# Kernel tuning notes

Hardware: AMD Instinct MI355X
Metric: run time of the kernel (lower is better)

The kernel has to match this reference:

```python
import jax, jax.numpy as jnp
import numpy as np

NUM_EXPERTS = 8
TOP_K = 2
HIDDEN = 2048
INTER = 7168
NUM_TOKENS = 8192


def setup_inputs() -> dict:
    key = jax.random.key(0)
    k0, k1, k2, k3, k4 = jax.random.split(key, 5)
    hidden_states = jax.random.normal(k0, (NUM_TOKENS, HIDDEN), dtype=jnp.float32)
    gate_w = jax.random.normal(k1, (NUM_EXPERTS, HIDDEN), dtype=jnp.float32) / 10.0
    w1 = jax.random.normal(k2, (NUM_EXPERTS, INTER, HIDDEN), dtype=jnp.float32) / 10.0
    w3 = jax.random.normal(k3, (NUM_EXPERTS, INTER, HIDDEN), dtype=jnp.float32) / 10.0
    w2 = jax.random.normal(k4, (NUM_EXPERTS, HIDDEN, INTER), dtype=jnp.float32) / 10.0
    return {"hidden_states": hidden_states, "gate_w": gate_w, "w1": w1, "w3": w3, "w2": w2}


def reference(hidden_states, gate_w, w1, w3, w2):
    x = hidden_states  # [T, H]
    num_experts = gate_w.shape[0]
    # router
    router_logits = x @ gate_w.T  # [T, E]
    probs = jax.nn.softmax(router_logits.astype(jnp.float32), axis=-1)
    top_w, top_i = jax.lax.top_k(probs, TOP_K)              # [T, K]
    top_w = top_w / jnp.sum(top_w, axis=-1, keepdims=True)  # renormalize
    top_w = top_w.astype(x.dtype)
    # dense [T, E] routing weight (0 for unselected experts)
    expert_ids = jnp.arange(num_experts)
    w_dense = jnp.sum(
        jnp.where(top_i[:, :, None] == expert_ids[None, None, :], top_w[:, :, None], 0.0),
        axis=1,
    )  # [T, E]
    out = jnp.zeros_like(x)
    for e in range(num_experts):
        g = jax.nn.silu(x @ w1[e].T) * (x @ w3[e].T)  # [T, I]
        out = out + w_dense[:, e:e + 1] * (g @ w2[e].T)
    return out
```

## Files before the change

### kernel.cpp

```cpp
#include <hip/hip_runtime.h>

#define NTOK 8192
#define HID 2048
#define ITR 7168
#define NE 8
#define BK32 32
#define TILE32 (128 * BK32)

typedef __attribute__((ext_vector_type(8))) short short8;
typedef __attribute__((ext_vector_type(8))) __bf16 bf16x8;
typedef __attribute__((ext_vector_type(4))) float f32x4;

__device__ __forceinline__ unsigned short f2bf(float f) {
  unsigned int u = __float_as_uint(f);
  u += 0x7FFFu + ((u >> 16) & 1u);
  return (unsigned short)(u >> 16);
}

__device__ __forceinline__ f32x4 mfma_bf16(short8 a, short8 b, f32x4 c) {
  union U { short8 s; bf16x8 b; };
  U ua; ua.s = a;
  U ub; ub.s = b;
  return __builtin_amdgcn_mfma_f32_16x16x32_bf16(ua.b, ub.b, c, 0, 0, 0);
}

typedef __attribute__((address_space(1))) const unsigned int g_u32;
typedef __attribute__((address_space(3))) unsigned int l_u32;

__device__ __forceinline__ void gload16(const unsigned short* src, unsigned short* dst) {
  __builtin_amdgcn_global_load_lds((g_u32*)src, (l_u32*)dst, 16, 0, 0);
}

__device__ __forceinline__ short8 read_frag32(const unsigned short* base, int row, int kelem) {
  int slot = ((row << 2) + (kelem >> 3)) ^ (row & 7);
  return *reinterpret_cast<const short8*>(reinterpret_cast<const char*>(base) + slot * 16);
}

__device__ __forceinline__ void slot_src(int s, int* row, int* c) {
  int r0 = ((s >> 2) ^ (s >> 4)) & 1;
  *row = ((s >> 2) & ~1) | r0;
  *c = ((s ^ r0) & 1) | ((((s >> 1) ^ (s >> 3)) & 1) << 1);
}

#define VMCNT(N) asm volatile("s_waitcnt vmcnt(" #N ")" ::: "memory")
#define BARRIER()                         \
  do {                                    \
    __builtin_amdgcn_s_barrier();         \
    asm volatile("" ::: "memory");        \
  } while (0)

__global__ __launch_bounds__(256) void moe_router(
    const float* __restrict__ x, const float* __restrict__ gw,
    int* __restrict__ cnt, int* __restrict__ pair_token, float* __restrict__ pair_w,
    int4* __restrict__ tok_ep) {
  int wave = threadIdx.x >> 6;
  int lane = threadIdx.x & 63;
  int t = blockIdx.x * 4 + wave;
  const float4* xr = reinterpret_cast<const float4*>(x + (size_t)t * HID);
  float acc[NE];
#pragma unroll
  for (int e = 0; e < NE; ++e) acc[e] = 0.f;
#pragma unroll
  for (int j = 0; j < 8; ++j) {
    int c = lane + 64 * j;
    float4 xv = xr[c];
#pragma unroll
    for (int e = 0; e < NE; ++e) {
      float4 gv = reinterpret_cast<const float4*>(gw + (size_t)e * HID)[c];
      acc[e] += xv.x * gv.x + xv.y * gv.y + xv.z * gv.z + xv.w * gv.w;
    }
  }
#pragma unroll
  for (int e = 0; e < NE; ++e) {
    float s = acc[e];
#pragma unroll
    for (int m = 32; m > 0; m >>= 1) s += __shfl_xor(s, m);
    acc[e] = s;
  }
  if (lane == 0) {
    int e0 = 0; float l0 = acc[0];
#pragma unroll
    for (int e = 1; e < NE; ++e) if (acc[e] > l0) { l0 = acc[e]; e0 = e; }
    int e1 = -1; float l1 = -3.0e38f;
#pragma unroll
    for (int e = 0; e < NE; ++e) if (e != e0 && acc[e] > l1) { l1 = acc[e]; e1 = e; }
    float z = __expf(l1 - l0);
    float w0 = 1.f / (1.f + z);
    float w1 = z / (1.f + z);
    int p0 = atomicAdd(&cnt[e0], 1);
    pair_token[e0 * NTOK + p0] = t;
    pair_w[e0 * NTOK + p0] = w0;
    int p1 = atomicAdd(&cnt[e1], 1);
    pair_token[e1 * NTOK + p1] = t;
    pair_w[e1 * NTOK + p1] = w1;
    tok_ep[t] = make_int4(e0, e1, p0, p1);
  }
}

__global__ void moe_scan(const int* __restrict__ cnt, int* __restrict__ base) {
  if (threadIdx.x == 0) {
    int s = 0;
#pragma unroll
    for (int e = 0; e < NE; ++e) { base[e] = s; s += cnt[e]; }
  }
}

__global__ __launch_bounds__(256) void moe_cvt(const float* __restrict__ src,
                                               unsigned short* __restrict__ dst) {
  size_t i = (size_t)blockIdx.x * 256 + threadIdx.x;
  const float4* p = reinterpret_cast<const float4*>(src) + i * 2;
  float4 a = p[0], b = p[1];
  union { unsigned short us[8]; short8 v; } u;
  u.us[0] = f2bf(a.x); u.us[1] = f2bf(a.y); u.us[2] = f2bf(a.z); u.us[3] = f2bf(a.w);
  u.us[4] = f2bf(b.x); u.us[5] = f2bf(b.y); u.us[6] = f2bf(b.z); u.us[7] = f2bf(b.w);
  reinterpret_cast<short8*>(dst)[i] = u.v;
}


__global__ __launch_bounds__(256, 2) void moe_gemm1_e(
    const unsigned short* __restrict__ xb, const unsigned short* __restrict__ w1b,
    const unsigned short* __restrict__ w3b, const int* __restrict__ cnt,
    const int* __restrict__ base, const int* __restrict__ pair_token,
    unsigned short* __restrict__ g) {
  int e = blockIdx.z;
  int n_e = cnt[e];
  int rowTile = blockIdx.x;
  if (rowTile * 128 >= n_e) return;
  int colTile = blockIdx.y;

  __shared__ unsigned short lds[3 * 3 * TILE32];

  int tid = threadIdx.x;
  int lane = tid & 63;
  int wv = tid >> 6;
  int wr = wv >> 1, wc = wv & 1;
  int lr = lane & 15;
  int lk = (lane >> 4) * 8;

  int slotP = e * NTOK + rowTile * 128;
  int slotG = base[e] + rowTile * 128;
  const unsigned short* w1e = w1b + (size_t)e * ITR * HID + (size_t)colTile * 128 * HID;
  const unsigned short* w3e = w3b + (size_t)e * ITR * HID + (size_t)colTile * 128 * HID;

  const unsigned short* a_s[2];
  const unsigned short* b1_s[2];
  const unsigned short* b3_s[2];
#pragma unroll
  for (int i = 0; i < 2; ++i) {
    int s = wv * 128 + i * 64 + lane;
    int row, c;
    slot_src(s, &row, &c);
    int tok = pair_token[slotP + ((rowTile * 128 + row < n_e) ? row : 0)];
    a_s[i] = xb + (size_t)tok * HID + c * 8;
    b1_s[i] = w1e + (size_t)row * HID + c * 8;
    b3_s[i] = w3e + (size_t)row * HID + c * 8;
  }

  f32x4 acc1[4][4], acc3[4][4];
#pragma unroll
  for (int m = 0; m < 4; ++m)
#pragma unroll
    for (int n = 0; n < 4; ++n) {
      acc1[m][n] = (f32x4){0.f, 0.f, 0.f, 0.f};
      acc3[m][n] = (f32x4){0.f, 0.f, 0.f, 0.f};
    }

#define STAGE1(buf, koff)                                                        \
  do {                                                                           \
    unsigned short* Lb = lds + (buf) * 3 * TILE32 + wv * 1024;                   \
    _Pragma("unroll") for (int i = 0; i < 2; ++i) {                              \
      gload16(a_s[i] + (koff), Lb + i * 512);                                    \
      gload16(b1_s[i] + (koff), Lb + TILE32 + i * 512);                          \
      gload16(b3_s[i] + (koff), Lb + 2 * TILE32 + i * 512);                      \
    }                                                                            \
  } while (0)

  const int nt = HID / BK32;
  STAGE1(0, 0);
  STAGE1(1, BK32);

  for (int t = 0; t < nt; ++t) {
    if (t + 1 < nt) VMCNT(6); else VMCNT(0);
    BARRIER();

    const unsigned short* A = lds + (t % 3) * 3 * TILE32;
    const unsigned short* B1 = A + TILE32;
    const unsigned short* B3 = A + 2 * TILE32;
    short8 av[4];
#pragma unroll
    for (int m = 0; m < 4; ++m) av[m] = read_frag32(A, wr * 64 + m * 16 + lr, lk);
#pragma unroll
    for (int n = 0; n < 4; ++n) {
      short8 b1v = read_frag32(B1, wc * 64 + n * 16 + lr, lk);
      short8 b3v = read_frag32(B3, wc * 64 + n * 16 + lr, lk);
#pragma unroll
      for (int m = 0; m < 4; ++m) {
        acc1[m][n] = mfma_bf16(av[m], b1v, acc1[m][n]);
        acc3[m][n] = mfma_bf16(av[m], b3v, acc3[m][n]);
      }
    }

    if (t + 2 < nt) STAGE1((t + 2) % 3, (t + 2) * BK32);
  }
#undef STAGE1

#pragma unroll
  for (int m = 0; m < 4; ++m) {
    int rbase = wr * 64 + m * 16 + ((lane >> 4) << 2);
#pragma unroll
    for (int r = 0; r < 4; ++r) {
      int rt = rbase + r;
      if (rowTile * 128 + rt < n_e) {
        unsigned short* grow = g + (size_t)(slotG + rt) * ITR + colTile * 128 + wc * 64;
#pragma unroll
        for (int n = 0; n < 4; ++n) {
          float h1 = acc1[m][n][r], h3 = acc3[m][n][r];
          float sl = h1 / (1.f + __expf(-h1));
          grow[n * 16 + lr] = f2bf(sl * h3);
        }
      }
    }
  }
}

__global__ __launch_bounds__(256, 2) void moe_gemm2_k(
    const unsigned short* __restrict__ g, const unsigned short* __restrict__ w2b,
    const int* __restrict__ cnt, const int* __restrict__ base,
    const float* __restrict__ pair_w, float* __restrict__ part) {
  int e = blockIdx.z;
  int n_e = cnt[e];
  int rowTile = blockIdx.x;
  if (rowTile * 128 >= n_e) return;
  int colTile = blockIdx.y;

  __shared__ unsigned short lds[3 * 3 * TILE32];

  int tid = threadIdx.x;
  int lane = tid & 63;
  int wv = tid >> 6;
  int wr = wv >> 1, wc = wv & 1;
  int lr = lane & 15;
  int lk = (lane >> 4) * 8;

  int slotP = e * NTOK + rowTile * 128;
  int slotG = base[e] + rowTile * 128;
  const unsigned short* w2e = w2b + (size_t)e * HID * ITR + (size_t)colTile * 256 * ITR;

  const unsigned short* a_s[2];
  const unsigned short* b0_s[2];
  const unsigned short* b1_s[2];
#pragma unroll
  for (int i = 0; i < 2; ++i) {
    int s = wv * 128 + i * 64 + lane;
    int row, c;
    slot_src(s, &row, &c);
    int rclamp = (rowTile * 128 + row < n_e) ? row : 0;
    a_s[i] = g + (size_t)(slotG + rclamp) * ITR + c * 8;
    b0_s[i] = w2e + (size_t)row * ITR + c * 8;
    b1_s[i] = w2e + (size_t)(128 + row) * ITR + c * 8;
  }

  f32x4 acc0[4][4], acc1[4][4];
#pragma unroll
  for (int m = 0; m < 4; ++m)
#pragma unroll
    for (int n = 0; n < 4; ++n) {
      acc0[m][n] = (f32x4){0.f, 0.f, 0.f, 0.f};
      acc1[m][n] = (f32x4){0.f, 0.f, 0.f, 0.f};
    }

#define STAGE2(buf, koff)                                                        \
  do {                                                                           \
    unsigned short* Lb = lds + (buf) * 3 * TILE32 + wv * 1024;                   \
    _Pragma("unroll") for (int i = 0; i < 2; ++i) {                              \
      gload16(a_s[i] + (koff), Lb + i * 512);                                    \
      gload16(b0_s[i] + (koff), Lb + TILE32 + i * 512);                          \
      gload16(b1_s[i] + (koff), Lb + 2 * TILE32 + i * 512);                      \
    }                                                                            \
  } while (0)

  const int nt = ITR / BK32;
  STAGE2(0, 0);
  STAGE2(1, BK32);

  for (int t = 0; t < nt; ++t) {
    if (t + 1 < nt) VMCNT(6); else VMCNT(0);
    BARRIER();

    const unsigned short* A = lds + (t % 3) * 3 * TILE32;
    const unsigned short* B0 = A + TILE32;
    const unsigned short* B1 = A + 2 * TILE32;
    short8 av[4];
#pragma unroll
    for (int m = 0; m < 4; ++m) av[m] = read_frag32(A, wr * 64 + m * 16 + lr, lk);
#pragma unroll
    for (int n = 0; n < 4; ++n) {
      short8 b0v = read_frag32(B0, wc * 64 + n * 16 + lr, lk);
      short8 b1v = read_frag32(B1, wc * 64 + n * 16 + lr, lk);
#pragma unroll
      for (int m = 0; m < 4; ++m) {
        acc0[m][n] = mfma_bf16(av[m], b0v, acc0[m][n]);
        acc1[m][n] = mfma_bf16(av[m], b1v, acc1[m][n]);
      }
    }

    if (t + 2 < nt) STAGE2((t + 2) % 3, (t + 2) * BK32);
  }
#undef STAGE2

#pragma unroll
  for (int m = 0; m < 4; ++m) {
    int rbase = wr * 64 + m * 16 + ((lane >> 4) << 2);
#pragma unroll
    for (int r = 0; r < 4; ++r) {
      int rt = rbase + r;
      if (rowTile * 128 + rt < n_e) {
        float wgt = pair_w[slotP + rt];
        float* prow = part + (size_t)(slotG + rt) * HID + colTile * 256 + wc * 64;
#pragma unroll
        for (int n = 0; n < 4; ++n) {
          prow[n * 16 + lr] = wgt * acc0[m][n][r];
          prow[128 + n * 16 + lr] = wgt * acc1[m][n][r];
        }
      }
    }
  }
}

__global__ __launch_bounds__(256) void moe_combine(
    const float* __restrict__ part, const int4* __restrict__ tok_ep,
    const int* __restrict__ base, float* __restrict__ out) {
  int t = blockIdx.x;
  int4 ep = tok_ep[t];
  int s0 = base[ep.x] + ep.z;
  int s1 = base[ep.y] + ep.w;
  const float4* p0 = reinterpret_cast<const float4*>(part + (size_t)s0 * HID);
  const float4* p1 = reinterpret_cast<const float4*>(part + (size_t)s1 * HID);
  float4* o = reinterpret_cast<float4*>(out + (size_t)t * HID);
#pragma unroll
  for (int i = 0; i < 2; ++i) {
    int idx = threadIdx.x + i * 256;
    float4 a = p0[idx], b = p1[idx];
    o[idx] = make_float4(a.x + b.x, a.y + b.y, a.z + b.z, a.w + b.w);
  }
}


extern "C" void kernel_launch(void* const* d_in, const int* in_sizes, int n_in,
                              void* d_out, int out_size, void* d_ws, size_t ws_size,
                              hipStream_t stream) {
  const float* x = (const float*)d_in[0];
  const float* gate_w = (const float*)d_in[1];
  const float* w1 = (const float*)d_in[2];
  const float* w3 = (const float*)d_in[3];
  const float* w2 = (const float*)d_in[4];
  float* out = (float*)d_out;

  char* ws = (char*)d_ws;
  const size_t WEL = (size_t)NE * ITR * HID;
  const size_t G_BYTES = (size_t)NTOK * 2 * ITR * 2;
  const size_t XB_BYTES = (size_t)NTOK * HID * 2;
  const size_t PAIR_BYTES = (size_t)NE * NTOK * 4;
  const size_t TOKEP_BYTES = (size_t)NTOK * 16;
  const size_t WB_BYTES = WEL * 2;

  unsigned short* g = (unsigned short*)ws;
  unsigned short* xb = (unsigned short*)(ws + G_BYTES);
  int* pair_token = (int*)(ws + G_BYTES + XB_BYTES);
  float* pair_w = (float*)(ws + G_BYTES + XB_BYTES + PAIR_BYTES);
  int4* tok_ep = (int4*)(ws + G_BYTES + XB_BYTES + 2 * PAIR_BYTES);
  int* cnt = (int*)(ws + G_BYTES + XB_BYTES + 2 * PAIR_BYTES + TOKEP_BYTES);
  int* base = cnt + NE;
  char* wbase = ws + G_BYTES + XB_BYTES + 2 * PAIR_BYTES + TOKEP_BYTES + 256;
  unsigned short* w1b = (unsigned short*)wbase;
  unsigned short* w3b = (unsigned short*)(wbase + WB_BYTES);
  unsigned short* w2b = (unsigned short*)(wbase + 2 * WB_BYTES);
  float* part = (float*)wbase;

  hipMemsetAsync(cnt, 0, 2 * NE * sizeof(int), stream);

  moe_router<<<NTOK / 4, 256, 0, stream>>>(x, gate_w, cnt, pair_token, pair_w, tok_ep);
  moe_scan<<<1, 64, 0, stream>>>(cnt, base);
  moe_cvt<<<(NTOK * HID) / 2048, 256, 0, stream>>>(x, xb);

  const int WGRID = (int)(WEL / 2048);
  moe_cvt<<<WGRID, 256, 0, stream>>>(w1, w1b);
  moe_cvt<<<WGRID, 256, 0, stream>>>(w3, w3b);
  moe_cvt<<<WGRID, 256, 0, stream>>>(w2, w2b);

  moe_gemm1_e<<<dim3(NTOK / 128, ITR / 128, NE), 256, 0, stream>>>(
      xb, w1b, w3b, cnt, base, pair_token, g);
  moe_gemm2_k<<<dim3(NTOK / 128, HID / 256, NE), 256, 0, stream>>>(
      g, w2b, cnt, base, pair_w, part);
  moe_combine<<<NTOK, 256, 0, stream>>>(part, tok_ep, base, out);
}
```

Measured before the change: 3.175 ms.

## Enlarge gemm1 tile to 256 rows with 8 waves and double-buffered BK64 pipeline

The gate/up GEMM kernel now uses 512-thread blocks covering 256 token rows by 128 columns. K is processed in 64-wide steps with two LDS buffers, and loads for the next step are interleaved between split-phase MFMA groups, each guarded by barriers. The goal is better weight reuse across more rows and fewer K-loop iterations. In exchange it uses more LDS per block, adds more barriers per iteration, and waits on VMCNT(0) every step, which may expose load latency.

```diff
diff --git a/kernel.cpp b/kernel.cpp
--- a/kernel.cpp
+++ b/kernel.cpp
@@ -116,8 +116,9 @@
   reinterpret_cast<short8*>(dst)[i] = u.v;
 }
 
-
-__global__ __launch_bounds__(256, 2) void moe_gemm1_e(
+#define G1P_BUF 32768
+
+__global__ __launch_bounds__(512, 2) void moe_gemm1_p(
     const unsigned short* __restrict__ xb, const unsigned short* __restrict__ w1b,
     const unsigned short* __restrict__ w3b, const int* __restrict__ cnt,
     const int* __restrict__ base, const int* __restrict__ pair_token,
@@ -125,35 +126,40 @@
   int e = blockIdx.z;
   int n_e = cnt[e];
   int rowTile = blockIdx.x;
-  if (rowTile * 128 >= n_e) return;
+  if (rowTile * 256 >= n_e) return;
   int colTile = blockIdx.y;
 
-  __shared__ unsigned short lds[3 * 3 * TILE32];
+  __shared__ unsigned short lds[2 * G1P_BUF];
 
   int tid = threadIdx.x;
   int lane = tid & 63;
   int wv = tid >> 6;
-  int wr = wv >> 1, wc = wv & 1;
+  int wr = wv >> 1;
+  int wc = wv & 1;
   int lr = lane & 15;
   int lk = (lane >> 4) * 8;
 
-  int slotP = e * NTOK + rowTile * 128;
-  int slotG = base[e] + rowTile * 128;
+  int slotP = e * NTOK + rowTile * 256;
+  int slotG = base[e] + rowTile * 256;
   const unsigned short* w1e = w1b + (size_t)e * ITR * HID + (size_t)colTile * 128 * HID;
   const unsigned short* w3e = w3b + (size_t)e * ITR * HID + (size_t)colTile * 128 * HID;
 
-  const unsigned short* a_s[2];
-  const unsigned short* b1_s[2];
-  const unsigned short* b3_s[2];
-#pragma unroll
-  for (int i = 0; i < 2; ++i) {
-    int s = wv * 128 + i * 64 + lane;
+  const unsigned short* aA[2];
+#pragma unroll
+  for (int j = 0; j < 2; ++j) {
+    int s = j * 512 + tid;
     int row, c;
     slot_src(s, &row, &c);
-    int tok = pair_token[slotP + ((rowTile * 128 + row < n_e) ? row : 0)];
-    a_s[i] = xb + (size_t)tok * HID + c * 8;
-    b1_s[i] = w1e + (size_t)row * HID + c * 8;
-    b3_s[i] = w3e + (size_t)row * HID + c * 8;
+    int tok = pair_token[slotP + ((rowTile * 256 + row < n_e) ? row : 0)];
+    aA[j] = xb + (size_t)tok * HID + c * 8;
+  }
+  const unsigned short* aB1;
+  const unsigned short* aB3;
+  {
+    int row, c;
+    slot_src(tid, &row, &c);
+    aB1 = w1e + (size_t)row * HID + c * 8;
+    aB3 = w3e + (size_t)row * HID + c * 8;
   }
 
   f32x4 acc1[4][4], acc3[4][4];
@@ -165,44 +171,72 @@
       acc3[m][n] = (f32x4){0.f, 0.f, 0.f, 0.f};
     }
 
-#define STAGE1(buf, koff)                                                        \
+#define STG_A(buf, t_, h_)                                                       \
   do {                                                                           \
-    unsigned short* Lb = lds + (buf) * 3 * TILE32 + wv * 1024;                   \
-    _Pragma("unroll") for (int i = 0; i < 2; ++i) {                              \
-      gload16(a_s[i] + (koff), Lb + i * 512);                                    \
-      gload16(b1_s[i] + (koff), Lb + TILE32 + i * 512);                          \
-      gload16(b3_s[i] + (koff), Lb + 2 * TILE32 + i * 512);                      \
-    }                                                                            \
+    unsigned short* Lb = lds + (buf) * G1P_BUF + (h_) * 8192;                    \
+    gload16(aA[0] + ((t_) * 64 + (h_) * 32), Lb + (wv * 64) * 8);                \
+    gload16(aA[1] + ((t_) * 64 + (h_) * 32), Lb + (512 + wv * 64) * 8);          \
   } while (0)
-
-  const int nt = HID / BK32;
-  STAGE1(0, 0);
-  STAGE1(1, BK32);
+#define STG_B(buf, t_, h_)                                                       \
+  do {                                                                           \
+    unsigned short* Lb = lds + (buf) * G1P_BUF + 16384 + (h_) * 4096;            \
+    gload16(aB1 + ((t_) * 64 + (h_) * 32), Lb + wv * 512);                       \
+    gload16(aB3 + ((t_) * 64 + (h_) * 32), Lb + 8192 + wv * 512);                \
+  } while (0)
+
+  const int nt = HID / 64;
+  STG_A(0, 0, 0); STG_A(0, 0, 1); STG_B(0, 0, 0); STG_B(0, 0, 1);
 
   for (int t = 0; t < nt; ++t) {
-    if (t + 1 < nt) VMCNT(6); else VMCNT(0);
-    BARRIER();
-
-    const unsigned short* A = lds + (t % 3) * 3 * TILE32;
-    const unsigned short* B1 = A + TILE32;
-    const unsigned short* B3 = A + 2 * TILE32;
-    short8 av[4];
-#pragma unroll
-    for (int m = 0; m < 4; ++m) av[m] = read_frag32(A, wr * 64 + m * 16 + lr, lk);
-#pragma unroll
-    for (int n = 0; n < 4; ++n) {
-      short8 b1v = read_frag32(B1, wc * 64 + n * 16 + lr, lk);
-      short8 b3v = read_frag32(B3, wc * 64 + n * 16 + lr, lk);
-#pragma unroll
-      for (int m = 0; m < 4; ++m) {
-        acc1[m][n] = mfma_bf16(av[m], b1v, acc1[m][n]);
-        acc3[m][n] = mfma_bf16(av[m], b3v, acc3[m][n]);
-      }
-    }
-
-    if (t + 2 < nt) STAGE1((t + 2) % 3, (t + 2) * BK32);
-  }
-#undef STAGE1
+    int cb = t & 1, nb = cb ^ 1;
+    VMCNT(0);
+    BARRIER();
+
+    const unsigned short* A0 = lds + cb * G1P_BUF;
+    const unsigned short* A1 = A0 + 8192;
+    const unsigned short* B1h0 = A0 + 16384;
+    const unsigned short* B1h1 = A0 + 20480;
+    const unsigned short* B3h0 = A0 + 24576;
+    const unsigned short* B3h1 = A0 + 28672;
+
+    short8 av[4], bv[4];
+#pragma unroll
+    for (int m = 0; m < 4; ++m) av[m] = read_frag32(A0, wr * 64 + m * 16 + lr, lk);
+#pragma unroll
+    for (int n = 0; n < 4; ++n) bv[n] = read_frag32(B1h0, wc * 64 + n * 16 + lr, lk);
+    BARRIER();
+    if (t + 1 < nt) { STG_A(nb, t + 1, 0); STG_A(nb, t + 1, 1); }
+#pragma unroll
+    for (int n = 0; n < 4; ++n)
+#pragma unroll
+      for (int m = 0; m < 4; ++m) acc1[m][n] = mfma_bf16(av[m], bv[n], acc1[m][n]);
+#pragma unroll
+    for (int n = 0; n < 4; ++n) bv[n] = read_frag32(B3h0, wc * 64 + n * 16 + lr, lk);
+    BARRIER();
+    if (t + 1 < nt) { STG_B(nb, t + 1, 0); STG_B(nb, t + 1, 1); }
+#pragma unroll
+    for (int n = 0; n < 4; ++n)
+#pragma unroll
+      for (int m = 0; m < 4; ++m) acc3[m][n] = mfma_bf16(av[m], bv[n], acc3[m][n]);
+#pragma unroll
+    for (int m = 0; m < 4; ++m) av[m] = read_frag32(A1, wr * 64 + m * 16 + lr, lk);
+#pragma unroll
+    for (int n = 0; n < 4; ++n) bv[n] = read_frag32(B1h1, wc * 64 + n * 16 + lr, lk);
+    BARRIER();
+#pragma unroll
+    for (int n = 0; n < 4; ++n)
+#pragma unroll
+      for (int m = 0; m < 4; ++m) acc1[m][n] = mfma_bf16(av[m], bv[n], acc1[m][n]);
+#pragma unroll
+    for (int n = 0; n < 4; ++n) bv[n] = read_frag32(B3h1, wc * 64 + n * 16 + lr, lk);
+    BARRIER();
+#pragma unroll
+    for (int n = 0; n < 4; ++n)
+#pragma unroll
+      for (int m = 0; m < 4; ++m) acc3[m][n] = mfma_bf16(av[m], bv[n], acc3[m][n]);
+  }
+#undef STG_A
+#undef STG_B
 
 #pragma unroll
   for (int m = 0; m < 4; ++m) {
@@ -210,7 +244,7 @@
 #pragma unroll
     for (int r = 0; r < 4; ++r) {
       int rt = rbase + r;
-      if (rowTile * 128 + rt < n_e) {
+      if (rowTile * 256 + rt < n_e) {
         unsigned short* grow = g + (size_t)(slotG + rt) * ITR + colTile * 128 + wc * 64;
 #pragma unroll
         for (int n = 0; n < 4; ++n) {
@@ -388,7 +422,7 @@
   moe_cvt<<<WGRID, 256, 0, stream>>>(w3, w3b);
   moe_cvt<<<WGRID, 256, 0, stream>>>(w2, w2b);
 
-  moe_gemm1_e<<<dim3(NTOK / 128, ITR / 128, NE), 256, 0, stream>>>(
+  moe_gemm1_p<<<dim3(NTOK / 256, ITR / 128, NE), 512, 0, stream>>>(
       xb, w1b, w3b, cnt, base, pair_token, g);
   moe_gemm2_k<<<dim3(NTOK / 128, HID / 256, NE), 256, 0, stream>>>(
       g, w2b, cnt, base, pair_w, part);
```

New measurement: 4.713 ms. 48.4% more time.
